# Optimization experiments

Measured on AMD Instinct MI355X. Metric: run time of the kernel, lower is better.

Reference implementation:

```python
import jax, jax.numpy as jnp
import numpy as np

NUM_USERS = 100000
NUM_BOOKS = 50000
HIDDEN = 128
USER_FEAT = 256
BOOK_FEAT = 256
E_PER_REL = 500000
NUM_LAYERS = 2


def setup_inputs() -> dict:
    key = jax.random.key(0)
    ks = jax.random.split(key, 10)
    user_x = jax.random.normal(ks[0], (NUM_USERS, USER_FEAT), dtype=jnp.float32)
    book_x = jax.random.normal(ks[1], (NUM_BOOKS, BOOK_FEAT), dtype=jnp.float32)
    user_W = jax.random.normal(ks[2], (HIDDEN, USER_FEAT), dtype=jnp.float32) * 0.05
    user_b = jax.random.normal(ks[3], (HIDDEN,), dtype=jnp.float32) * 0.05
    book_W = jax.random.normal(ks[4], (HIDDEN, BOOK_FEAT), dtype=jnp.float32) * 0.05
    book_b = jax.random.normal(ks[5], (HIDDEN,), dtype=jnp.float32) * 0.05
    # edge_index[0] = user indices, edge_index[1] = book indices
    rates_edge = jnp.stack([
        jax.random.randint(ks[6], (E_PER_REL,), 0, NUM_USERS),
        jax.random.randint(ks[7], (E_PER_REL,), 0, NUM_BOOKS)])
    implicit_edge = jnp.stack([
        jax.random.randint(ks[8], (E_PER_REL,), 0, NUM_USERS),
        jax.random.randint(ks[9], (E_PER_REL,), 0, NUM_BOOKS)])
    return {"user_x": user_x, "book_x": book_x, "user_W": user_W,
            "user_b": user_b, "book_W": book_W, "book_b": book_b,
            "rates_edge": rates_edge, "implicit_edge": implicit_edge}


def _lightgcn(user_x, book_x, user_W, user_b, book_W, book_b, rates_edge, implicit_edge):
    num_users = user_x.shape[0]
    num_nodes = num_users + book_x.shape[0]
    # input projections
    cu = user_x @ user_W.T + user_b  # [U, H]
    cb = book_x @ book_W.T + book_b  # [B, H]
    user_embeds = [cu]
    book_embeds = [cb]
    # build full directed edge list exactly as in the torch source
    all_edges = jnp.concatenate([rates_edge, implicit_edge], axis=1)  # [2, E]
    book_to_user = jnp.stack([all_edges[1] + num_users, all_edges[0]])
    full_edge = jnp.concatenate([all_edges, book_to_user], axis=1)  # [2, 2E]
    row, col = full_edge[0], full_edge[1]
    # symmetric degree normalization (edges fixed across layers)
    deg = jax.ops.segment_sum(jnp.ones(col.shape, dtype=cu.dtype), col,
                              num_segments=num_nodes)
    deg_inv_sqrt = jnp.where(deg > 0, jax.lax.rsqrt(jnp.maximum(deg, 1.0) * 0 + jnp.where(deg > 0, deg, 1.0)), 0.0)
    deg_inv_sqrt = jnp.where(deg > 0, jax.lax.rsqrt(jnp.where(deg > 0, deg, 1.0)), 0.0)
    norm = deg_inv_sqrt[row] * deg_inv_sqrt[col]  # [2E]
    for _ in range(NUM_LAYERS):
        x = jnp.concatenate([cu, cb], axis=0)  # [U+B, H]
        msg = x[row] * norm[:, None]           # gather + scale, [2E, H]
        out = jax.ops.segment_sum(msg, col, num_segments=num_nodes)  # scatter-add
        cu = out[:num_users]
        cb = out[num_users:]
        user_embeds.append(cu)
        book_embeds.append(cb)
    final_user = jnp.mean(jnp.stack(user_embeds), axis=0)
    final_book = jnp.mean(jnp.stack(book_embeds), axis=0)
    return final_user, final_book


def reference(user_x, book_x, user_W, user_b, book_W, book_b, rates_edge, implicit_edge):
    return _lightgcn(user_x, book_x, user_W, user_b, book_W, book_b,
                     rates_edge, implicit_edge)
```

## Files before the change

### kernel.cpp

```cpp
#include <hip/hip_runtime.h>

#define NUSERS 100000
#define NBOOKS 50000
#define HID 128
#define FEAT 256
#define EPR 500000
#define NEDGE (2 * EPR)

typedef __attribute__((ext_vector_type(8))) short bf16x8;
typedef __attribute__((ext_vector_type(4))) float f32x4;

__device__ __forceinline__ unsigned short f2bf(float f) {
  union { float f; unsigned u; } v; v.f = f;
  unsigned r = v.u + 0x7FFFu + ((v.u >> 16) & 1u);
  return (unsigned short)(r >> 16);
}
__device__ __forceinline__ float bf2f(unsigned short h) {
  union { unsigned u; float f; } v; v.u = ((unsigned)h) << 16;
  return v.f;
}

__global__ void cast_w(const float* __restrict__ w0, const float* __restrict__ w1,
                       unsigned short* __restrict__ o0, unsigned short* __restrict__ o1)
{
  int i = blockIdx.x * 256 + threadIdx.x;
  if (i < HID * FEAT) { o0[i] = f2bf(w0[i]); o1[i] = f2bf(w1[i]); }
}

__global__ __launch_bounds__(256) void gemm_all(
    const float* __restrict__ Xu, const float* __restrict__ Xb,
    const unsigned short* __restrict__ Wu, const unsigned short* __restrict__ Wb,
    const float* __restrict__ bu, const float* __restrict__ bb,
    unsigned short* __restrict__ cu0b, float* __restrict__ outb)
{
  const int UB = (NUSERS + 127) / 128;
  const bool isU = (int)blockIdx.x < UB;
  const float* __restrict__ X = isU ? Xu : Xb;
  const unsigned short* __restrict__ W = isU ? Wu : Wb;
  const float* __restrict__ bias = isU ? bu : bb;
  const int M  = isU ? NUSERS : NBOOKS;
  const int bm = (isU ? blockIdx.x : blockIdx.x - UB) * 128;

  const int tid  = threadIdx.x;
  const int lane = tid & 63;
  const int wv   = tid >> 6;
  const int l15  = lane & 15, l4 = lane >> 4;
  const int row0 = bm + wv * 32;

  int r[2]; bool rok[2];
#pragma unroll
  for (int mi = 0; mi < 2; ++mi) { r[mi] = row0 + mi * 16 + l15; rok[mi] = r[mi] < M; }

  f32x4 acc[2][8];
#pragma unroll
  for (int mi = 0; mi < 2; ++mi)
#pragma unroll
    for (int ni = 0; ni < 8; ++ni) acc[mi][ni] = (f32x4)0.f;

  float4 xa[2][2];
#pragma unroll
  for (int mi = 0; mi < 2; ++mi) {
    if (rok[mi]) {
      const float4* ap = reinterpret_cast<const float4*>(&X[(size_t)r[mi] * FEAT + l4 * 8]);
      xa[mi][0] = ap[0]; xa[mi][1] = ap[1];
    } else {
      xa[mi][0] = make_float4(0.f, 0.f, 0.f, 0.f);
      xa[mi][1] = make_float4(0.f, 0.f, 0.f, 0.f);
    }
  }

#pragma unroll
  for (int ks = 0; ks < 8; ++ks) {
    float4 xn[2][2];
    if (ks < 7) {
#pragma unroll
      for (int mi = 0; mi < 2; ++mi) {
        if (rok[mi]) {
          const float4* ap = reinterpret_cast<const float4*>(
              &X[(size_t)r[mi] * FEAT + (ks + 1) * 32 + l4 * 8]);
          xn[mi][0] = ap[0]; xn[mi][1] = ap[1];
        } else {
          xn[mi][0] = make_float4(0.f, 0.f, 0.f, 0.f);
          xn[mi][1] = make_float4(0.f, 0.f, 0.f, 0.f);
        }
      }
    }
    bf16x8 a[2];
#pragma unroll
    for (int mi = 0; mi < 2; ++mi) {
      bf16x8 av;
      av[0] = (short)f2bf(xa[mi][0].x); av[1] = (short)f2bf(xa[mi][0].y);
      av[2] = (short)f2bf(xa[mi][0].z); av[3] = (short)f2bf(xa[mi][0].w);
      av[4] = (short)f2bf(xa[mi][1].x); av[5] = (short)f2bf(xa[mi][1].y);
      av[6] = (short)f2bf(xa[mi][1].z); av[7] = (short)f2bf(xa[mi][1].w);
      a[mi] = av;
    }
#pragma unroll
    for (int ni = 0; ni < 8; ++ni) {
      int col = ni * 16 + l15;
      bf16x8 bfr = *reinterpret_cast<const bf16x8*>(&W[(size_t)col * FEAT + ks * 32 + l4 * 8]);
      acc[0][ni] = __builtin_amdgcn_mfma_f32_16x16x32_bf16(a[0], bfr, acc[0][ni], 0, 0, 0);
      acc[1][ni] = __builtin_amdgcn_mfma_f32_16x16x32_bf16(a[1], bfr, acc[1][ni], 0, 0, 0);
    }
    if (ks < 7) {
#pragma unroll
      for (int mi = 0; mi < 2; ++mi) { xa[mi][0] = xn[mi][0]; xa[mi][1] = xn[mi][1]; }
    }
  }

#pragma unroll
  for (int ni = 0; ni < 8; ++ni) {
    int col = ni * 16 + l15;
    float bj = bias[col];
#pragma unroll
    for (int mi = 0; mi < 2; ++mi) {
#pragma unroll
      for (int j = 0; j < 4; ++j) {
        int rr = row0 + mi * 16 + l4 * 4 + j;
        if (rr < M) {
          float vv = acc[mi][ni][j] + bj;
          if (isU) cu0b[(size_t)rr * HID + col] = f2bf(vv);
          else     outb[(size_t)rr * HID + col] = vv * (1.0f / 3.0f);
        }
      }
    }
  }
}

__device__ __forceinline__ void decode_edge(const int* __restrict__ rates,
                                            const int* __restrict__ impl,
                                            int i, int& u, int& bk)
{
  if (i < EPR) { u = rates[i]; bk = rates[EPR + i]; }
  else { int j = i - EPR; u = impl[j]; bk = impl[EPR + j]; }
}

__global__ void hist_kernel(const int* __restrict__ rates, const int* __restrict__ impl,
                            int* __restrict__ degu, int* __restrict__ cntb,
                            unsigned int* __restrict__ relpos)
{
  int i = blockIdx.x * blockDim.x + threadIdx.x;
  if (i >= NEDGE) return;
  int u, bk;
  decode_edge(rates, impl, i, u, bk);
  relpos[i] = (unsigned int)atomicAdd(&cntb[bk], 1);
  atomicAdd(&degu[u], 1);
}

__global__ void dis_kernel(const int* __restrict__ degu, const int* __restrict__ cntb,
                           float* __restrict__ dis)
{
  int i = blockIdx.x * blockDim.x + threadIdx.x;
  if (i < NUSERS) {
    int d = degu[i] + (i < NBOOKS ? cntb[i] : 0);
    dis[i] = (d > 0) ? rsqrtf((float)d) : 0.f;
  }
}

__global__ void fill_scatter(const int* __restrict__ rates, const int* __restrict__ impl,
                             const int* __restrict__ offs,
                             const unsigned int* __restrict__ relpos,
                             int* __restrict__ brow)
{
  int i = blockIdx.x * blockDim.x + threadIdx.x;
  if (i >= NEDGE) return;
  int u, bk;
  decode_edge(rates, impl, i, u, bk);
  brow[offs[bk] + (int)relpos[i]] = u;
}

__global__ __launch_bounds__(1024) void scan_blocks(const int* __restrict__ counts,
                                                    int* __restrict__ offs,
                                                    int* __restrict__ bsum, int N)
{
  __shared__ int buf[1024];
  int t = threadIdx.x;
  int i = blockIdx.x * 1024 + t;
  int v = (i < N) ? counts[i] : 0;
  buf[t] = v;
  __syncthreads();
  for (int off = 1; off < 1024; off <<= 1) {
    int x = (t >= off) ? buf[t - off] : 0;
    __syncthreads();
    buf[t] += x;
    __syncthreads();
  }
  int incl = buf[t];
  if (i < N) offs[i] = incl - v;
  if (t == 1023) bsum[blockIdx.x] = incl;
}

__global__ void scan_totals(const int* __restrict__ bsum, int* __restrict__ bpre,
                            int* __restrict__ offs, int nb, int N)
{
  if (threadIdx.x == 0 && blockIdx.x == 0) {
    int run = 0;
    for (int b = 0; b < nb; ++b) { bpre[b] = run; run += bsum[b]; }
    offs[N] = run;
  }
}

__global__ void add_prefix(int* __restrict__ offs, const int* __restrict__ bpre, int N)
{
  int i = blockIdx.x * blockDim.x + threadIdx.x;
  if (i < N) offs[i] += bpre[i >> 10];
}

__global__ __launch_bounds__(256) void pull1(const unsigned short* __restrict__ srcb,
    const int* __restrict__ offs, const int* __restrict__ brow,
    const float* __restrict__ dis, unsigned short* __restrict__ dstb)
{
  int c = (blockIdx.x << 2) + (threadIdx.x >> 6);
  if (c >= NBOOKS) return;
  const int lane = threadIdx.x & 63;
  const int g = lane >> 4, l = lane & 15;
  const int s = offs[c], e = offs[c + 1];

  float acc[8];
#pragma unroll
  for (int j = 0; j < 8; ++j) acc[j] = 0.f;

  int i = s + g;
  for (; i + 4 < e; i += 8) {
    int rr0 = brow[i], rr1 = brow[i + 4];
    float w0 = dis[rr0], w1 = dis[rr1];
    bf16x8 v0 = *reinterpret_cast<const bf16x8*>(&srcb[(size_t)rr0 * HID + l * 8]);
    bf16x8 v1 = *reinterpret_cast<const bf16x8*>(&srcb[(size_t)rr1 * HID + l * 8]);
#pragma unroll
    for (int j = 0; j < 8; ++j) acc[j] += w0 * bf2f((unsigned short)v0[j]);
#pragma unroll
    for (int j = 0; j < 8; ++j) acc[j] += w1 * bf2f((unsigned short)v1[j]);
  }
  if (i < e) {
    int rr = brow[i];
    float w = dis[rr];
    bf16x8 v = *reinterpret_cast<const bf16x8*>(&srcb[(size_t)rr * HID + l * 8]);
#pragma unroll
    for (int j = 0; j < 8; ++j) acc[j] += w * bf2f((unsigned short)v[j]);
  }

#pragma unroll
  for (int j = 0; j < 8; ++j) {
    acc[j] += __shfl_xor(acc[j], 16, 64);
    acc[j] += __shfl_xor(acc[j], 32, 64);
  }
  if (g == 0) {
    float db = dis[c];
    bf16x8 o;
#pragma unroll
    for (int j = 0; j < 8; ++j) o[j] = (short)f2bf(db * acc[j]);
    *reinterpret_cast<bf16x8*>(&dstb[(size_t)c * HID + l * 8]) = o;
  }
}

__global__ __launch_bounds__(256) void pull2_final(const unsigned short* __restrict__ h1b,
    const int* __restrict__ offs, const int* __restrict__ brow,
    const float* __restrict__ dis, const unsigned short* __restrict__ cu0b,
    float* __restrict__ outu)
{
  int c = (blockIdx.x << 2) + (threadIdx.x >> 6);
  if (c >= NBOOKS) return;
  const int lane = threadIdx.x & 63;
  const int g = lane >> 4, l = lane & 15;
  const int s = offs[c], e = offs[c + 1];

  float acc[8];
#pragma unroll
  for (int j = 0; j < 8; ++j) acc[j] = 0.f;

  int i = s + g;
  for (; i + 4 < e; i += 8) {
    int rr0 = brow[i], rr1 = brow[i + 4];
    int rc0 = rr0 < NBOOKS ? rr0 : 0;
    int rc1 = rr1 < NBOOKS ? rr1 : 0;
    float w0 = rr0 < NBOOKS ? dis[rr0] : 0.f;
    float w1 = rr1 < NBOOKS ? dis[rr1] : 0.f;
    bf16x8 v0 = *reinterpret_cast<const bf16x8*>(&h1b[(size_t)rc0 * HID + l * 8]);
    bf16x8 v1 = *reinterpret_cast<const bf16x8*>(&h1b[(size_t)rc1 * HID + l * 8]);
#pragma unroll
    for (int j = 0; j < 8; ++j) acc[j] += w0 * bf2f((unsigned short)v0[j]);
#pragma unroll
    for (int j = 0; j < 8; ++j) acc[j] += w1 * bf2f((unsigned short)v1[j]);
  }
  if (i < e) {
    int rr = brow[i];
    int rc = rr < NBOOKS ? rr : 0;
    float w = rr < NBOOKS ? dis[rr] : 0.f;
    bf16x8 v = *reinterpret_cast<const bf16x8*>(&h1b[(size_t)rc * HID + l * 8]);
#pragma unroll
    for (int j = 0; j < 8; ++j) acc[j] += w * bf2f((unsigned short)v[j]);
  }

#pragma unroll
  for (int j = 0; j < 8; ++j) {
    acc[j] += __shfl_xor(acc[j], 16, 64);
    acc[j] += __shfl_xor(acc[j], 32, 64);
  }
  if (g == 0) {
    float db = dis[c];
    size_t idx = (size_t)c * HID + l * 8;
    bf16x8 c0 = *reinterpret_cast<const bf16x8*>(&cu0b[idx]);
    bf16x8 h1 = *reinterpret_cast<const bf16x8*>(&h1b[idx]);
    float4 o0, o1;
    float r[8];
#pragma unroll
    for (int j = 0; j < 8; ++j)
      r[j] = (bf2f((unsigned short)c0[j]) + bf2f((unsigned short)h1[j]) + db * acc[j]) * (1.0f / 3.0f);
    o0 = make_float4(r[0], r[1], r[2], r[3]);
    o1 = make_float4(r[4], r[5], r[6], r[7]);
    *reinterpret_cast<float4*>(&outu[idx])     = o0;
    *reinterpret_cast<float4*>(&outu[idx + 4]) = o1;
  }
}

__global__ __launch_bounds__(256) void upper_users(const unsigned short* __restrict__ cu0b,
                                                   float* __restrict__ outu)
{
  size_t i2 = (size_t)blockIdx.x * 256 + threadIdx.x;
  size_t off2 = (size_t)NBOOKS * HID / 2;
  size_t idx = (off2 + i2) * 2;
  ushort2 v = *reinterpret_cast<const ushort2*>(&cu0b[idx]);
  float2 o;
  o.x = bf2f(v.x) * (1.0f / 3.0f);
  o.y = bf2f(v.y) * (1.0f / 3.0f);
  *reinterpret_cast<float2*>(&outu[idx]) = o;
}

extern "C" void kernel_launch(void* const* d_in, const int* in_sizes, int n_in,
                              void* d_out, int out_size, void* d_ws, size_t ws_size,
                              hipStream_t stream)
{
  const float* user_x = (const float*)d_in[0];
  const float* book_x = (const float*)d_in[1];
  const float* user_W = (const float*)d_in[2];
  const float* user_b = (const float*)d_in[3];
  const float* book_W = (const float*)d_in[4];
  const float* book_b = (const float*)d_in[5];
  const int*   rates  = (const int*)d_in[6];
  const int*   impl   = (const int*)d_in[7];

  float* out      = (float*)d_out;
  float* out_user = out;
  float* out_book = out + (size_t)NUSERS * HID;

  char* p = (char*)d_ws;
  auto carve = [&](size_t bytes) -> void* {
    void* r = (void*)p;
    p += (bytes + 255) & ~(size_t)255;
    return r;
  };
  unsigned short* cu0b   = (unsigned short*)carve((size_t)NUSERS * HID * 2);
  unsigned short* h1b    = (unsigned short*)carve((size_t)NBOOKS * HID * 2);
  unsigned short* wub    = (unsigned short*)carve((size_t)HID * FEAT * 2);
  unsigned short* wbb    = (unsigned short*)carve((size_t)HID * FEAT * 2);
  int*          degu   = (int*)carve((size_t)NUSERS * 4);
  int*          cntb   = (int*)carve((size_t)NBOOKS * 4);
  float*        dis    = (float*)carve((size_t)NUSERS * 4);
  int*          offs   = (int*)carve((size_t)(NBOOKS + 2) * 4);
  int*          bsum   = (int*)carve(256 * 4);
  int*          bpre   = (int*)carve(256 * 4);
  unsigned int* relpos = (unsigned int*)carve((size_t)NEDGE * 4);
  int*          brow   = (int*)carve((size_t)NEDGE * 4);

  hipMemsetAsync(degu, 0, (size_t)NUSERS * 4, stream);
  hipMemsetAsync(cntb, 0, (size_t)NBOOKS * 4, stream);

  cast_w<<<(HID * FEAT + 255) / 256, 256, 0, stream>>>(user_W, book_W, wub, wbb);
  const int UB = (NUSERS + 127) / 128, BB = (NBOOKS + 127) / 128;
  gemm_all<<<UB + BB, 256, 0, stream>>>(user_x, book_x, wub, wbb, user_b, book_b,
                                        cu0b, out_book);

  hist_kernel<<<(NEDGE + 255) / 256, 256, 0, stream>>>(rates, impl, degu, cntb, relpos);
  dis_kernel<<<(NUSERS + 255) / 256, 256, 0, stream>>>(degu, cntb, dis);

  const int nb = (NBOOKS + 1023) / 1024;
  scan_blocks<<<nb, 1024, 0, stream>>>(cntb, offs, bsum, NBOOKS);
  scan_totals<<<1, 64, 0, stream>>>(bsum, bpre, offs, nb, NBOOKS);
  add_prefix<<<(NBOOKS + 255) / 256, 256, 0, stream>>>(offs, bpre, NBOOKS);
  fill_scatter<<<(NEDGE + 255) / 256, 256, 0, stream>>>(rates, impl, offs, relpos, brow);

  upper_users<<<(NUSERS - NBOOKS) * HID / 512, 256, 0, stream>>>(cu0b, out_user);

  pull1<<<(NBOOKS + 3) / 4, 256, 0, stream>>>(cu0b, offs, brow, dis, h1b);
  pull2_final<<<(NBOOKS + 3) / 4, 256, 0, stream>>>(h1b, offs, brow, dis, cu0b, out_user);
}
```

Before: 304.9 us.

## Fuse edge histogram into GEMM launch, stage A tiles via LDS, drop upper_users

Measured after the change: 258.9 us. 1.18x faster.

```diff
diff --git a/kernel.cpp b/kernel.cpp
--- a/kernel.cpp
+++ b/kernel.cpp
@@ -7,6 +7,11 @@
 #define EPR 500000
 #define NEDGE (2 * EPR)
 
+#define UBLK ((NUSERS + 127) / 128)
+#define BBLK ((NBOOKS + 127) / 128)
+#define GEMM_BLOCKS (UBLK + BBLK)
+#define HIST_BLOCKS ((NEDGE + 1023) / 1024)
+
 typedef __attribute__((ext_vector_type(8))) short bf16x8;
 typedef __attribute__((ext_vector_type(4))) float f32x4;
 
@@ -27,29 +32,68 @@
   if (i < HID * FEAT) { o0[i] = f2bf(w0[i]); o1[i] = f2bf(w1[i]); }
 }
 
-__global__ __launch_bounds__(256) void gemm_all(
+__device__ __forceinline__ void decode_edge(const int* __restrict__ rates,
+                                            const int* __restrict__ impl,
+                                            int i, int& u, int& bk)
+{
+  if (i < EPR) { u = rates[i]; bk = rates[EPR + i]; }
+  else { int j = i - EPR; u = impl[j]; bk = impl[EPR + j]; }
+}
+
+__global__ __launch_bounds__(256) void gemm_hist(
     const float* __restrict__ Xu, const float* __restrict__ Xb,
     const unsigned short* __restrict__ Wu, const unsigned short* __restrict__ Wb,
     const float* __restrict__ bu, const float* __restrict__ bb,
-    unsigned short* __restrict__ cu0b, float* __restrict__ outb)
-{
-  const int UB = (NUSERS + 127) / 128;
-  const bool isU = (int)blockIdx.x < UB;
+    unsigned short* __restrict__ cu0b, float* __restrict__ outb,
+    float* __restrict__ outu,
+    const int* __restrict__ rates, const int* __restrict__ impl,
+    int* __restrict__ degu, int* __restrict__ cntb,
+    unsigned int* __restrict__ relpos)
+{
+  __shared__ float Abuf[2][128 * 32];
+  const int bid = blockIdx.x;
+  const int tid = threadIdx.x;
+
+  if (bid >= GEMM_BLOCKS) {
+    const int hb = bid - GEMM_BLOCKS;
+#pragma unroll
+    for (int q = 0; q < 4; ++q) {
+      int i = hb * 1024 + q * 256 + tid;
+      if (i < NEDGE) {
+        int u, bk;
+        decode_edge(rates, impl, i, u, bk);
+        relpos[i] = (unsigned int)atomicAdd(&cntb[bk], 1);
+        atomicAdd(&degu[u], 1);
+      }
+    }
+    return;
+  }
+
+  const bool isU = bid < UBLK;
   const float* __restrict__ X = isU ? Xu : Xb;
   const unsigned short* __restrict__ W = isU ? Wu : Wb;
   const float* __restrict__ bias = isU ? bu : bb;
   const int M  = isU ? NUSERS : NBOOKS;
-  const int bm = (isU ? blockIdx.x : blockIdx.x - UB) * 128;
-
-  const int tid  = threadIdx.x;
+  const int bm = (isU ? bid : bid - UBLK) * 128;
+
   const int lane = tid & 63;
   const int wv   = tid >> 6;
   const int l15  = lane & 15, l4 = lane >> 4;
-  const int row0 = bm + wv * 32;
-
-  int r[2]; bool rok[2];
-#pragma unroll
-  for (int mi = 0; mi < 2; ++mi) { r[mi] = row0 + mi * 16 + l15; rok[mi] = r[mi] < M; }
+  const int row0 = wv * 32;
+
+  auto stage = [&](int bf, int ks) {
+    const int k0 = ks * 32;
+#pragma unroll
+    for (int q = 0; q < 4; ++q) {
+      int o = q * 256 + tid;
+      int r = o >> 3;
+      int s = (o & 7) ^ (r & 7);
+      int gr = bm + r; if (gr > M - 1) gr = M - 1;
+      const float* src = &X[(size_t)gr * FEAT + k0 + s * 4];
+      float* dst = &Abuf[bf][(size_t)(q * 256 + wv * 64) * 4];
+      __builtin_amdgcn_global_load_lds(src, dst, 16, 0, 0);
+    }
+  };
 
   f32x4 acc[2][8];
 #pragma unroll
@@ -57,55 +101,43 @@
 #pragma unroll
     for (int ni = 0; ni < 8; ++ni) acc[mi][ni] = (f32x4)0.f;
 
-  float4 xa[2][2];
-#pragma unroll
-  for (int mi = 0; mi < 2; ++mi) {
-    if (rok[mi]) {
-      const float4* ap = reinterpret_cast<const float4*>(&X[(size_t)r[mi] * FEAT + l4 * 8]);
-      xa[mi][0] = ap[0]; xa[mi][1] = ap[1];
-    } else {
-      xa[mi][0] = make_float4(0.f, 0.f, 0.f, 0.f);
-      xa[mi][1] = make_float4(0.f, 0.f, 0.f, 0.f);
-    }
-  }
+  stage(0, 0);
 
 #pragma unroll
   for (int ks = 0; ks < 8; ++ks) {
-    float4 xn[2][2];
-    if (ks < 7) {
-#pragma unroll
-      for (int mi = 0; mi < 2; ++mi) {
-        if (rok[mi]) {
-          const float4* ap = reinterpret_cast<const float4*>(
-              &X[(size_t)r[mi] * FEAT + (ks + 1) * 32 + l4 * 8]);
-          xn[mi][0] = ap[0]; xn[mi][1] = ap[1];
-        } else {
-          xn[mi][0] = make_float4(0.f, 0.f, 0.f, 0.f);
-          xn[mi][1] = make_float4(0.f, 0.f, 0.f, 0.f);
-        }
-      }
-    }
-    bf16x8 a[2];
-#pragma unroll
-    for (int mi = 0; mi < 2; ++mi) {
-      bf16x8 av;
-      av[0] = (short)f2bf(xa[mi][0].x); av[1] = (short)f2bf(xa[mi][0].y);
-      av[2] = (short)f2bf(xa[mi][0].z); av[3] = (short)f2bf(xa[mi][0].w);
-      av[4] = (short)f2bf(xa[mi][1].x); av[5] = (short)f2bf(xa[mi][1].y);
-      av[6] = (short)f2bf(xa[mi][1].z); av[7] = (short)f2bf(xa[mi][1].w);
-      a[mi] = av;
-    }
+    if (ks < 7) stage((ks + 1) & 1, ks + 1);
+    __syncthreads();
+    const float* Ab = Abuf[ks & 1];
+
+    bf16x8 bfr[8];
 #pragma unroll
     for (int ni = 0; ni < 8; ++ni) {
       int col = ni * 16 + l15;
-      bf16x8 bfr = *reinterpret_cast<const bf16x8*>(&W[(size_t)col * FEAT + ks * 32 + l4 * 8]);
-      acc[0][ni] = __builtin_amdgcn_mfma_f32_16x16x32_bf16(a[0], bfr, acc[0][ni], 0, 0, 0);
-      acc[1][ni] = __builtin_amdgcn_mfma_f32_16x16x32_bf16(a[1], bfr, acc[1][ni], 0, 0, 0);
-    }
-    if (ks < 7) {
-#pragma unroll
-      for (int mi = 0; mi < 2; ++mi) { xa[mi][0] = xn[mi][0]; xa[mi][1] = xn[mi][1]; }
-    }
+      bfr[ni] = *reinterpret_cast<const bf16x8*>(&W[(size_t)col * FEAT + ks * 32 + l4 * 8]);
+    }
+
+    bf16x8 a[2];
+#pragma unroll
+    for (int mi = 0; mi < 2; ++mi) {
+      int rt = row0 + mi * 16 + l15;
+      int m7 = rt & 7;
+      int s0 = l4 * 2;
+      float4 x0 = *reinterpret_cast<const float4*>(&Ab[rt * 32 + ((s0)     ^ m7) * 4]);
+      float4 x1 = *reinterpret_cast<const float4*>(&Ab[rt * 32 + ((s0 + 1) ^ m7) * 4]);
+      bf16x8 av;
+      av[0] = (short)f2bf(x0.x); av[1] = (short)f2bf(x0.y);
+      av[2] = (short)f2bf(x0.z); av[3] = (short)f2bf(x0.w);
+      av[4] = (short)f2bf(x1.x); av[5] = (short)f2bf(x1.y);
+      av[6] = (short)f2bf(x1.z); av[7] = (short)f2bf(x1.w);
+      a[mi] = av;
+    }
+
+#pragma unroll
+    for (int ni = 0; ni < 8; ++ni) {
+      acc[0][ni] = __builtin_amdgcn_mfma_f32_16x16x32_bf16(a[0], bfr[ni], acc[0][ni], 0, 0, 0);
+      acc[1][ni] = __builtin_amdgcn_mfma_f32_16x16x32_bf16(a[1], bfr[ni], acc[1][ni], 0, 0, 0);
+    }
+    __syncthreads();
   }
 
 #pragma unroll
@@ -116,35 +148,19 @@
     for (int mi = 0; mi < 2; ++mi) {
 #pragma unroll
       for (int j = 0; j < 4; ++j) {
-        int rr = row0 + mi * 16 + l4 * 4 + j;
+        int rr = bm + row0 + mi * 16 + l4 * 4 + j;
         if (rr < M) {
           float vv = acc[mi][ni][j] + bj;
-          if (isU) cu0b[(size_t)rr * HID + col] = f2bf(vv);
-          else     outb[(size_t)rr * HID + col] = vv * (1.0f / 3.0f);
+          if (isU) {
+            cu0b[(size_t)rr * HID + col] = f2bf(vv);
+            if (rr >= NBOOKS) outu[(size_t)rr * HID + col] = vv * (1.0f / 3.0f);
+          } else {
+            outb[(size_t)rr * HID + col] = vv * (1.0f / 3.0f);
+          }
         }
       }
     }
   }
-}
-
-__device__ __forceinline__ void decode_edge(const int* __restrict__ rates,
-                                            const int* __restrict__ impl,
-                                            int i, int& u, int& bk)
-{
-  if (i < EPR) { u = rates[i]; bk = rates[EPR + i]; }
-  else { int j = i - EPR; u = impl[j]; bk = impl[EPR + j]; }
-}
-
-__global__ void hist_kernel(const int* __restrict__ rates, const int* __restrict__ impl,
-                            int* __restrict__ degu, int* __restrict__ cntb,
-                            unsigned int* __restrict__ relpos)
-{
-  int i = blockIdx.x * blockDim.x + threadIdx.x;
-  if (i >= NEDGE) return;
-  int u, bk;
-  decode_edge(rates, impl, i, u, bk);
-  relpos[i] = (unsigned int)atomicAdd(&cntb[bk], 1);
-  atomicAdd(&degu[u], 1);
 }
 
 __global__ void dis_kernel(const int* __restrict__ degu, const int* __restrict__ cntb,
@@ -301,29 +317,13 @@
     size_t idx = (size_t)c * HID + l * 8;
     bf16x8 c0 = *reinterpret_cast<const bf16x8*>(&cu0b[idx]);
     bf16x8 h1 = *reinterpret_cast<const bf16x8*>(&h1b[idx]);
-    float4 o0, o1;
     float r[8];
 #pragma unroll
     for (int j = 0; j < 8; ++j)
       r[j] = (bf2f((unsigned short)c0[j]) + bf2f((unsigned short)h1[j]) + db * acc[j]) * (1.0f / 3.0f);
-    o0 = make_float4(r[0], r[1], r[2], r[3]);
-    o1 = make_float4(r[4], r[5], r[6], r[7]);
-    *reinterpret_cast<float4*>(&outu[idx])     = o0;
-    *reinterpret_cast<float4*>(&outu[idx + 4]) = o1;
-  }
-}
-
-__global__ __launch_bounds__(256) void upper_users(const unsigned short* __restrict__ cu0b,
-                                                   float* __restrict__ outu)
-{
-  size_t i2 = (size_t)blockIdx.x * 256 + threadIdx.x;
-  size_t off2 = (size_t)NBOOKS * HID / 2;
-  size_t idx = (off2 + i2) * 2;
-  ushort2 v = *reinterpret_cast<const ushort2*>(&cu0b[idx]);
-  float2 o;
-  o.x = bf2f(v.x) * (1.0f / 3.0f);
-  o.y = bf2f(v.y) * (1.0f / 3.0f);
-  *reinterpret_cast<float2*>(&outu[idx]) = o;
+    *reinterpret_cast<float4*>(&outu[idx])     = make_float4(r[0], r[1], r[2], r[3]);
+    *reinterpret_cast<float4*>(&outu[idx + 4]) = make_float4(r[4], r[5], r[6], r[7]);
+  }
 }
 
 extern "C" void kernel_launch(void* const* d_in, const int* in_sizes, int n_in,
@@ -366,11 +366,11 @@
   hipMemsetAsync(cntb, 0, (size_t)NBOOKS * 4, stream);
 
   cast_w<<<(HID * FEAT + 255) / 256, 256, 0, stream>>>(user_W, book_W, wub, wbb);
-  const int UB = (NUSERS + 127) / 128, BB = (NBOOKS + 127) / 128;
-  gemm_all<<<UB + BB, 256, 0, stream>>>(user_x, book_x, wub, wbb, user_b, book_b,
-                                        cu0b, out_book);
-
-  hist_kernel<<<(NEDGE + 255) / 256, 256, 0, stream>>>(rates, impl, degu, cntb, relpos);
+
+  gemm_hist<<<GEMM_BLOCKS + HIST_BLOCKS, 256, 0, stream>>>(
+      user_x, book_x, wub, wbb, user_b, book_b,
+      cu0b, out_book, out_user, rates, impl, degu, cntb, relpos);
+
   dis_kernel<<<(NUSERS + 255) / 256, 256, 0, stream>>>(degu, cntb, dis);
 
   const int nb = (NBOOKS + 1023) / 1024;
@@ -379,8 +379,6 @@
   add_prefix<<<(NBOOKS + 255) / 256, 256, 0, stream>>>(offs, bpre, NBOOKS);
   fill_scatter<<<(NEDGE + 255) / 256, 256, 0, stream>>>(rates, impl, offs, relpos, brow);
 
-  upper_users<<<(NUSERS - NBOOKS) * HID / 512, 256, 0, stream>>>(cu0b, out_user);
-
   pull1<<<(NBOOKS + 3) / 4, 256, 0, stream>>>(cu0b, offs, brow, dis, h1b);
   pull2_final<<<(NBOOKS + 3) / 4, 256, 0, stream>>>(h1b, offs, brow, dis, cu0b, out_user);
 }
```
